# Kernel tuning notes

Hardware: AMD Instinct MI355X
Metric: run time of the kernel (lower is better)

## Reference

```python
import jax, jax.numpy as jnp
import numpy as np
from jax import lax

B, T, C = 8, 1025, 512
HEADS = 8
CACHE = 256          # int(dim * cache_ratio)
CLS = 1
L = 256              # gr_cache memory length
H = W = 32           # sqrt(T - CLS)
EPS = 1e-5


def setup_inputs() -> dict:
    key = jax.random.key(0)
    ks = jax.random.split(key, 40)
    def w(k, shape, scale=0.02):
        return jax.random.normal(k, shape, dtype=jnp.float32) * scale
    inp = {}
    inp['x'] = jax.random.normal(ks[0], (B, T, C), dtype=jnp.float32)
    inp['gr_cache'] = jax.random.normal(ks[1], (1, L, CACHE), dtype=jnp.float32)
    # self-attention (dim=512) params, weights stored (in, out)
    inp['Wq1'] = w(ks[2], (C, C)); inp['bq1'] = jnp.zeros((C,), jnp.float32)
    inp['Wk1'] = w(ks[3], (C, C)); inp['bk1'] = jnp.zeros((C,), jnp.float32)
    inp['Wv1'] = w(ks[4], (C, C)); inp['bv1'] = jnp.zeros((C,), jnp.float32)
    inp['Wo1'] = w(ks[5], (C, C)); inp['bo1'] = jnp.zeros((C,), jnp.float32)
    # memory attention (dim=cache_dim=256) params
    inp['Wq2'] = w(ks[6], (CACHE, CACHE)); inp['bq2'] = jnp.zeros((CACHE,), jnp.float32)
    inp['Wk2'] = w(ks[7], (CACHE, CACHE)); inp['bk2'] = jnp.zeros((CACHE,), jnp.float32)
    inp['Wv2'] = w(ks[8], (CACHE, CACHE)); inp['bv2'] = jnp.zeros((CACHE,), jnp.float32)
    inp['Wo2'] = w(ks[9], (CACHE, CACHE)); inp['bo2'] = jnp.zeros((CACHE,), jnp.float32)
    # GRU-style gate linears: in = 2*cache_dim, out = cache_dim
    inp['Wr'] = w(ks[10], (2 * CACHE, CACHE)); inp['br'] = jnp.zeros((CACHE,), jnp.float32)
    inp['Wz'] = w(ks[11], (2 * CACHE, CACHE)); inp['bz'] = jnp.zeros((CACHE,), jnp.float32)
    inp['Wa'] = w(ks[12], (2 * CACHE, CACHE)); inp['ba'] = jnp.zeros((CACHE,), jnp.float32)
    # LayerNorm(cache_dim)
    inp['gamma'] = jnp.ones((CACHE,), jnp.float32)
    inp['beta'] = jnp.zeros((CACHE,), jnp.float32)
    # per-head gate logits, init to -1 as in the module
    inp['lam'] = jnp.full((HEADS,), -1.0, dtype=jnp.float32)
    # grouped conv pos-emb: Conv2d(512, 512, k=3, groups=CACHE) -> (O=512, I/g=2, 3, 3)
    inp['conv_w'] = w(ks[13], (C, C // CACHE, 3, 3))
    inp['conv_b'] = jnp.zeros((C,), jnp.float32)
    return inp


def _mha(q_in, kv_in, Wq, bq, Wk, bk, Wv, bv, Wo, bo):
    Bq, Tq, D = q_in.shape
    Tk = kv_in.shape[1]
    dh = D // HEADS
    q = (q_in @ Wq + bq).reshape(Bq, Tq, HEADS, dh)
    k = (kv_in @ Wk + bk).reshape(Bq, Tk, HEADS, dh)
    v = (kv_in @ Wv + bv).reshape(Bq, Tk, HEADS, dh)
    s = jnp.einsum('bqhd,bkhd->bhqk', q, k) * (1.0 / np.sqrt(dh)).astype(np.float32)
    a = jax.nn.softmax(s, axis=-1)
    o = jnp.einsum('bhqk,bkhd->bqhd', a, v).reshape(Bq, Tq, D)
    return o @ Wo + bo


def reference(x, gr_cache, Wq1, bq1, Wk1, bk1, Wv1, bv1, Wo1, bo1,
              Wq2, bq2, Wk2, bk2, Wv2, bv2, Wo2, bo2,
              Wr, br, Wz, bz, Wa, ba, gamma, beta, lam, conv_w, conv_b):
    B_, T_, C_ = x.shape
    # ---- spatial positional embedding (faithful to torch view->permute quirk) ----
    tok = x[:, CLS:, :].reshape(B_, H, W, C_).transpose(0, 3, 1, 2)   # (B, C, H, W)
    pos = lax.conv_general_dilated(tok, conv_w, (1, 1), 'SAME',
                                   feature_group_count=CACHE,
                                   dimension_numbers=('NCHW', 'OIHW', 'NCHW'))
    pos = pos + conv_b[None, :, None, None]
    pos = pos.reshape(B_, C_, T_ - CLS).transpose(0, 2, 1)            # (B, T-1, C)
    pos = jnp.concatenate([jnp.zeros((B_, CLS, C_), pos.dtype), pos], axis=1)
    # ---- self attention ----
    x_self = _mha(x, x, Wq1, bq1, Wk1, bk1, Wv1, bv1, Wo1, bo1)       # (B, T, C)
    x_self_h = x_self.reshape(B_, T_, HEADS, C_ // HEADS)
    # ---- GRU-style gated cache update ----
    gr = jnp.broadcast_to(gr_cache, (B_, L, CACHE))
    x_summary = x_self[:, :, :CACHE]
    idx = (jnp.arange(L) * T_) // L                                   # nearest interpolate T -> L
    x_summary = x_summary[:, idx, :]                                  # (B, L, CACHE)
    cat = jnp.concatenate([gr, x_summary], axis=-1)
    reset = jax.nn.sigmoid(cat @ Wr + br)
    z = jax.nn.sigmoid(cat @ Wz + bz)
    cat2 = jnp.concatenate([reset * gr, x_summary], axis=-1)
    add = jax.nn.gelu(cat2 @ Wa + ba, approximate=False)
    mu = add.mean(-1, keepdims=True)
    var = ((add - mu) ** 2).mean(-1, keepdims=True)
    add = (add - mu) / jnp.sqrt(var + EPS) * gamma + beta             # LayerNorm
    gr_new = z * add + (1.0 - z) * gr
    # ---- memory attention on first cache_dim channels ----
    x_mem = _mha(x[:, :, :CACHE], gr_new, Wq2, bq2, Wk2, bk2, Wv2, bv2, Wo2, bo2)
    x_mem = x_mem.reshape(B_, T_, HEADS, CACHE // HEADS)
    # ---- per-head alpha blend with zero-padded mem branch ----
    alpha = jax.nn.sigmoid(lam).reshape(1, 1, HEADS, 1)
    pad = jnp.zeros((B_, T_, HEADS, (C_ - CACHE) // HEADS), x.dtype)
    out = (alpha * jnp.concatenate([x_mem, pad], axis=-1)
           + (1.0 - alpha) * x_self_h).reshape(B_, T_, C_) + pos
    return out
```

## Files before the change

kernel.cpp:

```cpp
#include <hip/hip_runtime.h>
#include <math.h>

typedef unsigned short u16;
typedef unsigned int u32;
typedef __attribute__((ext_vector_type(8))) short short8;
typedef __attribute__((ext_vector_type(4))) short short4v;
typedef __attribute__((ext_vector_type(4))) float f32x4;

constexpr int Bc = 8;
constexpr int Tt = 1025;
constexpr int Cc = 512;
constexpr int Hn = 8;
constexpr int CA = 256;
constexpr int Ll = 256;

#if __has_builtin(__builtin_amdgcn_exp2f)
#define EXP2F __builtin_amdgcn_exp2f
#else
#define EXP2F exp2f
#endif

__device__ __forceinline__ u16 f2bf(float f) {
  u32 u = __builtin_bit_cast(u32, f);
  u = (u + 0x7FFFu + ((u >> 16) & 1u)) >> 16;
  return (u16)u;
}
__device__ __forceinline__ u32 pack2f(float lo, float hi) {
  const u32 a = __builtin_bit_cast(u32, hi) + 0x8000u;
  const u32 b = __builtin_bit_cast(u32, lo) + 0x8000u;
  return __builtin_amdgcn_perm(a, b, 0x07060302u);
}

struct WC { const float* s; u16* d; int N; int tot; int kshift; };
struct WCP { WC w[11]; };

__global__ void wcast_k(WCP p) {
  const WC a = p.w[blockIdx.y];
  const int kmask = (1 << a.kshift) - 1;
  for (int idx = blockIdx.x * 256 + threadIdx.x; idx < a.tot; idx += gridDim.x * 256) {
    const int k = idx & kmask;
    const int n = idx >> a.kshift;
    a.d[idx] = f2bf(a.s[(size_t)k * a.N + n]);
  }
}

__global__ void xcast_k(const float* __restrict__ x, u16* __restrict__ xb, int n) {
  const int i = blockIdx.x * 256 + threadIdx.x;
  if (i < n) xb[i] = f2bf(x[i]);
}

enum { EP_NONE = 0, EP_SIGMOID = 1, EP_GELU = 2 };

template <int OUTBF, int ACT>
__global__ __launch_bounds__(256) void gemm_mfma(
    const u16* __restrict__ A, int lda,
    const u16* __restrict__ Wt,
    const float* __restrict__ bias,
    void* __restrict__ Cout,
    int M, int N, int K, float oscale)
{
  __shared__ u16 As[128][32];
  __shared__ u16 Bs[128][32];
  const int tid = threadIdx.x;
  const int m0 = blockIdx.y * 128, n0 = blockIdx.x * 128;
  const int ln = tid & 15, quad = (tid >> 4) & 3, wv = tid >> 6;
  const int wm = (wv & 1) * 64, wn = (wv >> 1) * 64;
  const int sr = tid >> 1;
  const int sk = (tid & 1) * 16;

  f32x4 zf = {0.f, 0.f, 0.f, 0.f};
  f32x4 acc[4][4];
  #pragma unroll
  for (int i = 0; i < 4; i++)
    #pragma unroll
    for (int j = 0; j < 4; j++) acc[i][j] = zf;

  const short8 z8 = {0, 0, 0, 0, 0, 0, 0, 0};

  for (int k0 = 0; k0 < K; k0 += 32) {
    const int gm = m0 + sr;
    short8 a0 = z8, a1 = z8;
    if (gm < M) {
      const u16* p = A + (size_t)gm * lda + k0 + sk;
      a0 = *(const short8*)p;
      a1 = *(const short8*)(p + 8);
    }
    *(short8*)&As[sr][sk] = a0;
    *(short8*)&As[sr][sk + 8] = a1;
    {
      const u16* q = Wt + (size_t)(n0 + sr) * K + k0 + sk;
      *(short8*)&Bs[sr][sk] = *(const short8*)q;
      *(short8*)&Bs[sr][sk + 8] = *(const short8*)(q + 8);
    }
    __syncthreads();

    short8 af[4], bf[4];
    #pragma unroll
    for (int i = 0; i < 4; i++) af[i] = *(const short8*)&As[wm + i * 16 + ln][quad * 8];
    #pragma unroll
    for (int j = 0; j < 4; j++) bf[j] = *(const short8*)&Bs[wn + j * 16 + ln][quad * 8];
    #pragma unroll
    for (int i = 0; i < 4; i++)
      #pragma unroll
      for (int j = 0; j < 4; j++)
        acc[i][j] = __builtin_amdgcn_mfma_f32_16x16x32_bf16(af[i], bf[j], acc[i][j], 0, 0, 0);
    __syncthreads();
  }

  float bj[4];
  #pragma unroll
  for (int j = 0; j < 4; j++) bj[j] = bias[n0 + wn + j * 16 + ln];

  #pragma unroll
  for (int i = 0; i < 4; i++) {
    #pragma unroll
    for (int r = 0; r < 4; r++) {
      const int gm = m0 + wm + i * 16 + quad * 4 + r;
      if (gm >= M) continue;
      #pragma unroll
      for (int j = 0; j < 4; j++) {
        float v = (acc[i][j][r] + bj[j]) * oscale;
        if (ACT == EP_SIGMOID)   v = 1.f / (1.f + __expf(-v));
        else if (ACT == EP_GELU) v = 0.5f * v * (1.f + erff(v * 0.70710678118654752f));
        const size_t off = (size_t)gm * N + n0 + wn + j * 16 + ln;
        if (OUTBF) ((u16*)Cout)[off] = f2bf(v);
        else       ((float*)Cout)[off] = v;
      }
    }
  }
}

template <int DH>
__global__ __launch_bounds__(128) void attn_mfma(
    const u16* __restrict__ Qp, const u16* __restrict__ Kp,
    const u16* __restrict__ Vp, u16* __restrict__ Op,
    int Tq, int Tk, int qbs, int kbs)
{
  constexpr int RS = Hn * DH;
  constexpr int MK = DH / 8 - 1;
  constexpr int NC = DH / 32;
  constexpr int NM = DH / 16;

  __shared__ u16 Ks[32 * DH];
  __shared__ u16 Vt[DH * 32];
  __shared__ u16 Pb[2 * 32 * 32];

  const int b = blockIdx.y >> 3, h = blockIdx.y & 7;
  const int q0 = blockIdx.x * 64;
  const int tid = threadIdx.x;
  const int wv = tid >> 6;
  const int lane = tid & 63;
  const int ln = lane & 15, quad = lane >> 4;

  const u16* Qb = Qp + (size_t)b * qbs + h * DH;
  const u16* Kb = Kp + (size_t)b * kbs + h * DH;
  const u16* Vb = Vp + (size_t)b * kbs + h * DH;
  u16* Ob = Op + (size_t)b * qbs + h * DH;

  const short8 z8 = {0, 0, 0, 0, 0, 0, 0, 0};
  const f32x4 zf = {0.f, 0.f, 0.f, 0.f};

  short8 qf[2][NC];
  #pragma unroll
  for (int qs = 0; qs < 2; qs++) {
    const int gq = q0 + wv * 32 + qs * 16 + ln;
    #pragma unroll
    for (int c = 0; c < NC; c++) {
      if (gq < Tq) qf[qs][c] = *(const short8*)(Qb + (size_t)gq * RS + c * 32 + quad * 8);
      else         qf[qs][c] = z8;
    }
  }

  f32x4 oacc[2][NM];
  float lsum[2] = {0.f, 0.f};
  #pragma unroll
  for (int qs = 0; qs < 2; qs++)
    #pragma unroll
    for (int c = 0; c < NM; c++) oacc[qs][c] = zf;

  const int nfull = Tk >> 5;
  const int nit = (Tk + 31) >> 5;

  for (int it = 0; it < nit; it++) {
    const int k0 = it << 5;
    const bool full = (it < nfull);
    __syncthreads();

    {
      const int r = tid >> 2;
      const int gk = k0 + r;
      if (DH == 64) {
        const u16* p = Kb + (size_t)gk * RS + (tid & 3) * 16;
        short8 a = z8, b2 = z8;
        if (full || gk < Tk) { a = *(const short8*)p; b2 = *(const short8*)(p + 8); }
        const int g0 = (((tid & 3) * 2) ^ (r & 7));
        const int g1 = (((tid & 3) * 2 + 1) ^ (r & 7));
        *(short8*)&Ks[r * 64 + g0 * 8] = a;
        *(short8*)&Ks[r * 64 + g1 * 8] = b2;
      } else {
        const u16* p = Kb + (size_t)gk * RS + (tid & 3) * 8;
        short8 a = z8;
        if (full || gk < Tk) a = *(const short8*)p;
        const int g0 = ((tid & 3) ^ (r & 3));
        *(short8*)&Ks[r * 32 + g0 * 8] = a;
      }
    }
    {
      const int vd0 = (tid & 15) * (DH / 16);
      const int vk = (tid >> 4) * 4;
      const int gb = vk >> 3, off = vk & 7;
      short4v vrow[4];
      #pragma unroll
      for (int i2 = 0; i2 < 4; i2++) {
        const int gk = k0 + vk + i2;
        short4v t = {0, 0, 0, 0};
        if (DH == 64) {
          if (full || gk < Tk) t = *(const short4v*)(Vb + (size_t)gk * RS + vd0);
        } else {
          if (full || gk < Tk) {
            ushort2 u = *(const ushort2*)(Vb + (size_t)gk * RS + vd0);
            t[0] = (short)u.x; t[1] = (short)u.y;
          }
        }
        vrow[i2] = t;
      }
      #pragma unroll
      for (int i = 0; i < DH / 16; i++) {
        const int d = vd0 + i;
        const int h2 = (d ^ (d >> 3)) & 3;
        short4v w = {vrow[0][i], vrow[1][i], vrow[2][i], vrow[3][i]};
        *(short4v*)&Vt[d * 32 + ((gb ^ h2) << 3) + off] = w;
      }
    }
    __syncthreads();

    short8 kf[2][NC];
    #pragma unroll
    for (int kc = 0; kc < 2; kc++) {
      const int r = kc * 16 + ln;
      #pragma unroll
      for (int c = 0; c < NC; c++) {
        const int g = (4 * c + quad) ^ (r & MK);
        kf[kc][c] = *(const short8*)&Ks[r * DH + g * 8];
      }
    }

    #pragma unroll
    for (int qs = 0; qs < 2; qs++) {
      #pragma unroll
      for (int kc = 0; kc < 2; kc++) {
        f32x4 s = zf;
        #pragma unroll
        for (int c = 0; c < NC; c++)
          s = __builtin_amdgcn_mfma_f32_16x16x32_bf16(kf[kc][c], qf[qs][c], s, 0, 0, 0);
        float p0, p1, p2, p3;
        if (full) {
          p0 = EXP2F(s[0]); p1 = EXP2F(s[1]); p2 = EXP2F(s[2]); p3 = EXP2F(s[3]);
        } else {
          const int kb = k0 + kc * 16 + quad * 4;
          p0 = (kb + 0 < Tk) ? EXP2F(s[0]) : 0.f;
          p1 = (kb + 1 < Tk) ? EXP2F(s[1]) : 0.f;
          p2 = (kb + 2 < Tk) ? EXP2F(s[2]) : 0.f;
          p3 = (kb + 3 < Tk) ? EXP2F(s[3]) : 0.f;
        }
        lsum[qs] += (p0 + p1) + (p2 + p3);
        short4v pw;
        ((u32*)&pw)[0] = pack2f(p0, p1);
        ((u32*)&pw)[1] = pack2f(p2, p3);
        const int q = qs * 16 + ln;
        const int g = ((kc * 2 + (quad >> 1)) ^ (ln & 3)) & 3;
        *(short4v*)&Pb[wv * 1024 + q * 32 + (g << 3) + (quad & 1) * 4] = pw;
      }
    }

    short8 pf2[2];
    #pragma unroll
    for (int qs = 0; qs < 2; qs++) {
      const int q = qs * 16 + ln;
      const int g = quad ^ (ln & 3);
      pf2[qs] = *(const short8*)&Pb[wv * 1024 + q * 32 + g * 8];
    }
    #pragma unroll
    for (int c = 0; c < NM; c++) {
      const int d = c * 16 + ln;
      const int g = quad ^ ((d ^ (d >> 3)) & 3);
      const short8 vf = *(const short8*)&Vt[d * 32 + g * 8];
      #pragma unroll
      for (int qs = 0; qs < 2; qs++)
        oacc[qs][c] = __builtin_amdgcn_mfma_f32_16x16x32_bf16(pf2[qs], vf, oacc[qs][c], 0, 0, 0);
    }
  }

  float lq[2];
  #pragma unroll
  for (int qs = 0; qs < 2; qs++) {
    float t = lsum[qs];
    t += __shfl_xor(t, 16);
    t += __shfl_xor(t, 32);
    lq[qs] = t;
  }
  #pragma unroll
  for (int qs = 0; qs < 2; qs++) {
    #pragma unroll
    for (int r = 0; r < 4; r++) {
      const float linv = 1.f / __shfl(lq[qs], quad * 4 + r);
      const int gq = q0 + wv * 32 + qs * 16 + quad * 4 + r;
      if (gq >= Tq) continue;
      #pragma unroll
      for (int c = 0; c < NM; c++)
        Ob[(size_t)gq * RS + c * 16 + ln] = f2bf(oacc[qs][c][r] * linv);
    }
  }
}

__global__ __launch_bounds__(256) void conv_combine(
    const float* __restrict__ x, const float* __restrict__ cw,
    const float* __restrict__ cb, const float* __restrict__ x_self,
    const float* __restrict__ x_mem, const float* __restrict__ lam,
    float* __restrict__ out)
{
  const int bh = blockIdx.x;
  const int b = bh >> 5, hh = bh & 31;
  const int c = (blockIdx.y << 8) + threadIdx.x;
  const int ci = c & ~1;
  const int dd = c & 63;
  const int h8 = c >> 6;
  const float alpha = 1.f / (1.f + __expf(-lam[h8]));
  const float bias = cb[c];

  float wgt[2][9];
  #pragma unroll
  for (int ch = 0; ch < 2; ch++)
    #pragma unroll
    for (int k = 0; k < 9; k++) wgt[ch][k] = cw[c * 18 + ch * 9 + k];

  const float* xrow[3];
  bool rv[3];
  #pragma unroll
  for (int r = 0; r < 3; r++) {
    const int h2 = hh + r - 1;
    rv[r] = (unsigned)h2 < 32u;
    xrow[r] = x + ((size_t)(b * Tt) + 1 + h2 * 32) * Cc + ci;
  }

  float2 win[3][3];
  #pragma unroll
  for (int r = 0; r < 3; r++) {
    win[r][0] = make_float2(0.f, 0.f);
    win[r][1] = rv[r] ? *(const float2*)(xrow[r]) : make_float2(0.f, 0.f);
  }

  const size_t bT = (size_t)b * Tt;
  for (int w = 0; w < 32; w++) {
    #pragma unroll
    for (int r = 0; r < 3; r++)
      win[r][2] = (rv[r] && w + 1 < 32) ? *(const float2*)(xrow[r] + (w + 1) * Cc)
                                        : make_float2(0.f, 0.f);
    float pos = bias;
    #pragma unroll
    for (int r = 0; r < 3; r++)
      #pragma unroll
      for (int col = 0; col < 3; col++) {
        pos += win[r][col].x * wgt[0][r * 3 + col];
        pos += win[r][col].y * wgt[1][r * 3 + col];
      }
    const size_t bt = bT + 1 + hh * 32 + w;
    const float mem = (dd < 32) ? x_mem[bt * 256 + h8 * 32 + dd] : 0.f;
    out[bt * 512 + c] = pos + alpha * mem + (1.f - alpha) * x_self[bt * 512 + c];
    #pragma unroll
    for (int r = 0; r < 3; r++) { win[r][0] = win[r][1]; win[r][1] = win[r][2]; }
  }

  if (hh == 0) {
    const float mem = (dd < 32) ? x_mem[bT * 256 + h8 * 32 + dd] : 0.f;
    out[bT * 512 + c] = alpha * mem + (1.f - alpha) * x_self[bT * 512 + c];
  }
}

__global__ void build_cat(const float* __restrict__ gr_cache,
                          const float* __restrict__ x_self,
                          u16* __restrict__ cat)
{
  const int idx = blockIdx.x * 256 + threadIdx.x;
  if (idx >= Bc * Ll * 512) return;
  const int k = idx & 511;
  const int bi = idx >> 9;
  const int i = bi & 255;
  const int b = bi >> 8;
  float v;
  if (k < 256) v = gr_cache[i * 256 + k];
  else         v = x_self[((size_t)(b * Tt + 4 * i)) * Cc + (k - 256)];
  cat[idx] = f2bf(v);
}

__global__ void build_cat2(const float* __restrict__ gr_cache,
                           const float* __restrict__ reset,
                           u16* __restrict__ cat)
{
  const int idx = blockIdx.x * 256 + threadIdx.x;
  if (idx >= Bc * Ll * 256) return;
  const int k = idx & 255;
  const int bi = idx >> 8;
  const int i = bi & 255;
  cat[(size_t)bi * 512 + k] = f2bf(gr_cache[i * 256 + k] * reset[idx]);
}

__device__ inline float block_sum256(float v, float* red)
{
  #pragma unroll
  for (int o = 32; o >= 1; o >>= 1) v += __shfl_down(v, o);
  const int wid = threadIdx.x >> 6;
  if ((threadIdx.x & 63) == 0) red[wid] = v;
  __syncthreads();
  const float t = red[0] + red[1] + red[2] + red[3];
  __syncthreads();
  return t;
}

__global__ __launch_bounds__(256) void ln_gate(
    const float* __restrict__ add_raw, const float* __restrict__ z,
    const float* __restrict__ gr_cache, const float* __restrict__ gamma,
    const float* __restrict__ beta, u16* __restrict__ gr_new)
{
  __shared__ float red[4];
  const int bi = blockIdx.x;
  const int i = bi & 255;
  const int c = threadIdx.x;
  const float v = add_raw[(size_t)bi * 256 + c];
  const float mu = block_sum256(v, red) * (1.f / 256.f);
  const float dv = v - mu;
  const float var = block_sum256(dv * dv, red) * (1.f / 256.f);
  const float nrm = dv * rsqrtf(var + 1e-5f) * gamma[c] + beta[c];
  const float zz = z[(size_t)bi * 256 + c];
  gr_new[(size_t)bi * 256 + c] = f2bf(zz * nrm + (1.f - zz) * gr_cache[i * 256 + c]);
}

extern "C" void kernel_launch(void* const* d_in, const int* in_sizes, int n_in,
                              void* d_out, int out_size, void* d_ws, size_t ws_size,
                              hipStream_t stream)
{
  const float* x        = (const float*)d_in[0];
  const float* gr_cache = (const float*)d_in[1];
  const float* Wq1 = (const float*)d_in[2];  const float* bq1 = (const float*)d_in[3];
  const float* Wk1 = (const float*)d_in[4];  const float* bk1 = (const float*)d_in[5];
  const float* Wv1 = (const float*)d_in[6];  const float* bv1 = (const float*)d_in[7];
  const float* Wo1 = (const float*)d_in[8];  const float* bo1 = (const float*)d_in[9];
  const float* Wq2 = (const float*)d_in[10]; const float* bq2 = (const float*)d_in[11];
  const float* Wk2 = (const float*)d_in[12]; const float* bk2 = (const float*)d_in[13];
  const float* Wv2 = (const float*)d_in[14]; const float* bv2 = (const float*)d_in[15];
  const float* Wo2 = (const float*)d_in[16]; const float* bo2 = (const float*)d_in[17];
  const float* Wr  = (const float*)d_in[18]; const float* br  = (const float*)d_in[19];
  const float* Wz  = (const float*)d_in[20]; const float* bz  = (const float*)d_in[21];
  const float* Wa  = (const float*)d_in[22]; const float* ba  = (const float*)d_in[23];
  const float* gamma = (const float*)d_in[24];
  const float* beta  = (const float*)d_in[25];
  const float* lam   = (const float*)d_in[26];
  const float* conv_w = (const float*)d_in[27];
  const float* conv_b = (const float*)d_in[28];
  float* out = (float*)d_out;

  const int M1 = Bc * Tt;
  const int M2 = Bc * Ll;
  const size_t BTC = (size_t)Bc * Tt * Cc;
  const size_t BLA = (size_t)Bc * Ll * CA;
  const size_t BL2 = (size_t)Bc * Ll * 512;

  char* W = (char*)d_ws;
  u16*   xb     = (u16*)(W + 0);
  u16*   q1     = (u16*)(W + 8396800);
  u16*   k1     = (u16*)(W + 16793600);
  u16*   v1     = (u16*)(W + 25190400);
  u16*   att1   = (u16*)(W + 33587200);
  float* x_self = (float*)(W + 41984000);
  u16*   wtb    = (u16*)(W + 58777600);
  u16*   cat    = (u16*)(W + 8396800);
  float* rg     = (float*)(W + 10493952);
  float* zg     = (float*)(W + 12591104);
  float* addr_  = (float*)(W + 14688256);
  u16*   gr_new = (u16*)(W + 16785408);
  u16*   k2     = (u16*)(W + 17833984);
  u16*   v2     = (u16*)(W + 18882560);
  u16*   q2     = (u16*)(W + 19931136);
  u16*   att2   = (u16*)(W + 24129536);
  float* x_mem  = (float*)(W + 28327936);

  u16* Wq1t = wtb + 0;       u16* Wk1t = wtb + 262144;  u16* Wv1t = wtb + 524288;
  u16* Wo1t = wtb + 786432;  u16* Wrt  = wtb + 1048576; u16* Wzt  = wtb + 1179648;
  u16* Wat  = wtb + 1310720; u16* Wq2t = wtb + 1441792; u16* Wk2t = wtb + 1507328;
  u16* Wv2t = wtb + 1572864; u16* Wo2t = wtb + 1638400;

  const dim3 blk(256);
  const int ew_btc = (int)((BTC + 255) / 256);

  {
    WCP p;
    const float* ws_[11] = {Wq1, Wk1, Wv1, Wo1, Wr, Wz, Wa, Wq2, Wk2, Wv2, Wo2};
    u16* wd_[11] = {Wq1t, Wk1t, Wv1t, Wo1t, Wrt, Wzt, Wat, Wq2t, Wk2t, Wv2t, Wo2t};
    const int Kk[11] = {512,512,512,512,512,512,512,256,256,256,256};
    const int Nn[11] = {512,512,512,512,256,256,256,256,256,256,256};
    for (int i = 0; i < 11; i++) {
      p.w[i].s = ws_[i]; p.w[i].d = wd_[i]; p.w[i].N = Nn[i];
      p.w[i].tot = Kk[i] * Nn[i];
      p.w[i].kshift = (Kk[i] == 512) ? 9 : 8;
    }
    wcast_k<<<dim3(64, 11), blk, 0, stream>>>(p);
  }
  xcast_k<<<ew_btc, blk, 0, stream>>>(x, xb, (int)BTC);

  const dim3 g512(4, 65), g256m1(2, 65), g256m2(2, 16);
  gemm_mfma<1, EP_NONE><<<g512, blk, 0, stream>>>(xb, 512, Wq1t, bq1, q1, M1, 512, 512,
                                                  0.18033688011112042f);
  gemm_mfma<1, EP_NONE><<<g512, blk, 0, stream>>>(xb, 512, Wk1t, bk1, k1, M1, 512, 512, 1.f);
  gemm_mfma<1, EP_NONE><<<g512, blk, 0, stream>>>(xb, 512, Wv1t, bv1, v1, M1, 512, 512, 1.f);
  attn_mfma<64><<<dim3(17, 64), dim3(128), 0, stream>>>(q1, k1, v1, att1, Tt, Tt,
                                                        Tt * 512, Tt * 512);
  gemm_mfma<0, EP_NONE><<<g512, blk, 0, stream>>>(att1, 512, Wo1t, bo1, x_self, M1, 512, 512, 1.f);

  build_cat<<<(int)((BL2 + 255) / 256), blk, 0, stream>>>(gr_cache, x_self, cat);
  gemm_mfma<0, EP_SIGMOID><<<g256m2, blk, 0, stream>>>(cat, 512, Wrt, br, rg, M2, 256, 512, 1.f);
  gemm_mfma<0, EP_SIGMOID><<<g256m2, blk, 0, stream>>>(cat, 512, Wzt, bz, zg, M2, 256, 512, 1.f);
  build_cat2<<<(int)((BLA + 255) / 256), blk, 0, stream>>>(gr_cache, rg, cat);
  gemm_mfma<0, EP_GELU><<<g256m2, blk, 0, stream>>>(cat, 512, Wat, ba, addr_, M2, 256, 512, 1.f);
  ln_gate<<<M2, blk, 0, stream>>>(addr_, zg, gr_cache, gamma, beta, gr_new);

  gemm_mfma<1, EP_NONE><<<g256m1, blk, 0, stream>>>(xb, 512, Wq2t, bq2, q2, M1, 256, 256,
                                                    0.25503490664918414f);
  gemm_mfma<1, EP_NONE><<<g256m2, blk, 0, stream>>>(gr_new, 256, Wk2t, bk2, k2, M2, 256, 256, 1.f);
  gemm_mfma<1, EP_NONE><<<g256m2, blk, 0, stream>>>(gr_new, 256, Wv2t, bv2, v2, M2, 256, 256, 1.f);
  attn_mfma<32><<<dim3(17, 64), dim3(128), 0, stream>>>(q2, k2, v2, att2, Tt, Ll,
                                                        Tt * 256, Ll * 256);
  gemm_mfma<0, EP_NONE><<<g256m1, blk, 0, stream>>>(att2, 256, Wo2t, bo2, x_mem, M1, 256, 256, 1.f);

  conv_combine<<<dim3(Bc * 32, 2), blk, 0, stream>>>(x, conv_w, conv_b, x_self,
                                                     x_mem, lam, out);
}
```

Before: 397.2 us.

## Fuse QKV/Q2, R/Z, K2/V2 GEMMs; cast x in-GEMM; drop K smem staging

```diff
diff --git a/kernel.cpp b/kernel.cpp
--- a/kernel.cpp
+++ b/kernel.cpp
@@ -31,7 +31,7 @@
   return __builtin_amdgcn_perm(a, b, 0x07060302u);
 }
 
-struct WC { const float* s; u16* d; int N; int tot; int kshift; };
+struct WC { const float* s; u16* d; int sN; int sK; int kshift; int tot; };
 struct WCP { WC w[11]; };
 
 __global__ void wcast_k(WCP p) {
@@ -40,24 +40,26 @@
   for (int idx = blockIdx.x * 256 + threadIdx.x; idx < a.tot; idx += gridDim.x * 256) {
     const int k = idx & kmask;
     const int n = idx >> a.kshift;
-    a.d[idx] = f2bf(a.s[(size_t)k * a.N + n]);
-  }
-}
-
-__global__ void xcast_k(const float* __restrict__ x, u16* __restrict__ xb, int n) {
-  const int i = blockIdx.x * 256 + threadIdx.x;
-  if (i < n) xb[i] = f2bf(x[i]);
+    a.d[idx] = (k < a.sK) ? f2bf(a.s[(size_t)k * a.sN + n]) : (u16)0;
+  }
 }
 
 enum { EP_NONE = 0, EP_SIGMOID = 1, EP_GELU = 2 };
 
-template <int OUTBF, int ACT>
+struct GemmEpi {
+  const float* bias[4];
+  int start[4];
+  float scale[4];
+  int nreg;
+};
+
+template <int AF32, int OUTBF, int ACT>
 __global__ __launch_bounds__(256) void gemm_mfma(
-    const u16* __restrict__ A, int lda,
+    const void* __restrict__ Av, int lda,
     const u16* __restrict__ Wt,
-    const float* __restrict__ bias,
+    GemmEpi epi,
     void* __restrict__ Cout,
-    int M, int N, int K, float oscale)
+    int M, int N, int K)
 {
   __shared__ u16 As[128][32];
   __shared__ u16 Bs[128][32];
@@ -81,9 +83,25 @@
     const int gm = m0 + sr;
     short8 a0 = z8, a1 = z8;
     if (gm < M) {
-      const u16* p = A + (size_t)gm * lda + k0 + sk;
-      a0 = *(const short8*)p;
-      a1 = *(const short8*)(p + 8);
+      if (AF32) {
+        const float* p = (const float*)Av + (size_t)gm * lda + k0 + sk;
+        const float4 f0 = *(const float4*)(p + 0);
+        const float4 f1 = *(const float4*)(p + 4);
+        const float4 f2 = *(const float4*)(p + 8);
+        const float4 f3 = *(const float4*)(p + 12);
+        ((u32*)&a0)[0] = pack2f(f0.x, f0.y);
+        ((u32*)&a0)[1] = pack2f(f0.z, f0.w);
+        ((u32*)&a0)[2] = pack2f(f1.x, f1.y);
+        ((u32*)&a0)[3] = pack2f(f1.z, f1.w);
+        ((u32*)&a1)[0] = pack2f(f2.x, f2.y);
+        ((u32*)&a1)[1] = pack2f(f2.z, f2.w);
+        ((u32*)&a1)[2] = pack2f(f3.x, f3.y);
+        ((u32*)&a1)[3] = pack2f(f3.z, f3.w);
+      } else {
+        const u16* p = (const u16*)Av + (size_t)gm * lda + k0 + sk;
+        a0 = *(const short8*)p;
+        a1 = *(const short8*)(p + 8);
+      }
     }
     *(short8*)&As[sr][sk] = a0;
     *(short8*)&As[sr][sk + 8] = a1;
@@ -107,9 +125,16 @@
     __syncthreads();
   }
 
+  int ri = 0;
+  #pragma unroll
+  for (int i = 1; i < 4; i++)
+    if (i < epi.nreg && epi.start[i] <= n0) ri = i;
+  const float* bp = epi.bias[ri] - epi.start[ri];
+  const float sc = epi.scale[ri];
+
   float bj[4];
   #pragma unroll
-  for (int j = 0; j < 4; j++) bj[j] = bias[n0 + wn + j * 16 + ln];
+  for (int j = 0; j < 4; j++) bj[j] = bp[n0 + wn + j * 16 + ln];
 
   #pragma unroll
   for (int i = 0; i < 4; i++) {
@@ -119,7 +144,7 @@
       if (gm >= M) continue;
       #pragma unroll
       for (int j = 0; j < 4; j++) {
-        float v = (acc[i][j][r] + bj[j]) * oscale;
+        float v = (acc[i][j][r] + bj[j]) * sc;
         if (ACT == EP_SIGMOID)   v = 1.f / (1.f + __expf(-v));
         else if (ACT == EP_GELU) v = 0.5f * v * (1.f + erff(v * 0.70710678118654752f));
         const size_t off = (size_t)gm * N + n0 + wn + j * 16 + ln;
@@ -134,15 +159,12 @@
 __global__ __launch_bounds__(128) void attn_mfma(
     const u16* __restrict__ Qp, const u16* __restrict__ Kp,
     const u16* __restrict__ Vp, u16* __restrict__ Op,
-    int Tq, int Tk, int qbs, int kbs)
-{
-  constexpr int RS = Hn * DH;
-  constexpr int MK = DH / 8 - 1;
+    int Tq, int Tk, int qbs, int kbs, int obs, int qrs, int krs, int ors)
+{
   constexpr int NC = DH / 32;
   constexpr int NM = DH / 16;
 
-  __shared__ u16 Ks[32 * DH];
-  __shared__ u16 Vt[DH * 32];
+  __shared__ u16 Vt[2][DH * 32];
   __shared__ u16 Pb[2 * 32 * 32];
 
   const int b = blockIdx.y >> 3, h = blockIdx.y & 7;
@@ -155,7 +177,7 @@
   const u16* Qb = Qp + (size_t)b * qbs + h * DH;
   const u16* Kb = Kp + (size_t)b * kbs + h * DH;
   const u16* Vb = Vp + (size_t)b * kbs + h * DH;
-  u16* Ob = Op + (size_t)b * qbs + h * DH;
+  u16* Ob = Op + (size_t)b * obs + h * DH;
 
   const short8 z8 = {0, 0, 0, 0, 0, 0, 0, 0};
   const f32x4 zf = {0.f, 0.f, 0.f, 0.f};
@@ -166,7 +188,7 @@
     const int gq = q0 + wv * 32 + qs * 16 + ln;
     #pragma unroll
     for (int c = 0; c < NC; c++) {
-      if (gq < Tq) qf[qs][c] = *(const short8*)(Qb + (size_t)gq * RS + c * 32 + quad * 8);
+      if (gq < Tq) qf[qs][c] = *(const short8*)(Qb + (size_t)gq * qrs + c * 32 + quad * 8);
       else         qf[qs][c] = z8;
     }
   }
@@ -177,6 +199,10 @@
   for (int qs = 0; qs < 2; qs++)
     #pragma unroll
     for (int c = 0; c < NM; c++) oacc[qs][c] = zf;
+
+  const int vd0 = (tid & 15) * (DH / 16);
+  const int vk = (tid >> 4) * 4;
+  const int gb = vk >> 3, off = vk & 7;
 
   const int nfull = Tk >> 5;
   const int nit = (Tk + 31) >> 5;
@@ -184,41 +210,39 @@
   for (int it = 0; it < nit; it++) {
     const int k0 = it << 5;
     const bool full = (it < nfull);
-    __syncthreads();
+    u16* vt = &Vt[it & 1][0];
+
+    short8 kf[2][NC];
+    if (full) {
+      #pragma unroll
+      for (int kc = 0; kc < 2; kc++)
+        #pragma unroll
+        for (int c = 0; c < NC; c++)
+          kf[kc][c] = *(const short8*)(Kb + (size_t)(k0 + kc * 16 + ln) * krs
+                                          + c * 32 + quad * 8);
+    } else {
+      #pragma unroll
+      for (int kc = 0; kc < 2; kc++)
+        #pragma unroll
+        for (int c = 0; c < NC; c++) {
+          const int row = k0 + kc * 16 + ln;
+          kf[kc][c] = (row < Tk)
+              ? *(const short8*)(Kb + (size_t)row * krs + c * 32 + quad * 8)
+              : z8;
+        }
+    }
 
     {
-      const int r = tid >> 2;
-      const int gk = k0 + r;
-      if (DH == 64) {
-        const u16* p = Kb + (size_t)gk * RS + (tid & 3) * 16;
-        short8 a = z8, b2 = z8;
-        if (full || gk < Tk) { a = *(const short8*)p; b2 = *(const short8*)(p + 8); }
-        const int g0 = (((tid & 3) * 2) ^ (r & 7));
-        const int g1 = (((tid & 3) * 2 + 1) ^ (r & 7));
-        *(short8*)&Ks[r * 64 + g0 * 8] = a;
-        *(short8*)&Ks[r * 64 + g1 * 8] = b2;
-      } else {
-        const u16* p = Kb + (size_t)gk * RS + (tid & 3) * 8;
-        short8 a = z8;
-        if (full || gk < Tk) a = *(const short8*)p;
-        const int g0 = ((tid & 3) ^ (r & 3));
-        *(short8*)&Ks[r * 32 + g0 * 8] = a;
-      }
-    }
-    {
-      const int vd0 = (tid & 15) * (DH / 16);
-      const int vk = (tid >> 4) * 4;
-      const int gb = vk >> 3, off = vk & 7;
       short4v vrow[4];
       #pragma unroll
       for (int i2 = 0; i2 < 4; i2++) {
         const int gk = k0 + vk + i2;
         short4v t = {0, 0, 0, 0};
         if (DH == 64) {
-          if (full || gk < Tk) t = *(const short4v*)(Vb + (size_t)gk * RS + vd0);
+          if (full || gk < Tk) t = *(const short4v*)(Vb + (size_t)gk * krs + vd0);
         } else {
           if (full || gk < Tk) {
-            ushort2 u = *(const ushort2*)(Vb + (size_t)gk * RS + vd0);
+            ushort2 u = *(const ushort2*)(Vb + (size_t)gk * krs + vd0);
             t[0] = (short)u.x; t[1] = (short)u.y;
           }
         }
@@ -229,21 +253,10 @@
         const int d = vd0 + i;
         const int h2 = (d ^ (d >> 3)) & 3;
         short4v w = {vrow[0][i], vrow[1][i], vrow[2][i], vrow[3][i]};
-        *(short4v*)&Vt[d * 32 + ((gb ^ h2) << 3) + off] = w;
+        *(short4v*)&vt[d * 32 + ((gb ^ h2) << 3) + off] = w;
       }
     }
     __syncthreads();
-
-    short8 kf[2][NC];
-    #pragma unroll
-    for (int kc = 0; kc < 2; kc++) {
-      const int r = kc * 16 + ln;
-      #pragma unroll
-      for (int c = 0; c < NC; c++) {
-        const int g = (4 * c + quad) ^ (r & MK);
-        kf[kc][c] = *(const short8*)&Ks[r * DH + g * 8];
-      }
-    }
 
     #pragma unroll
     for (int qs = 0; qs < 2; qs++) {
@@ -284,7 +297,7 @@
     for (int c = 0; c < NM; c++) {
       const int d = c * 16 + ln;
       const int g = quad ^ ((d ^ (d >> 3)) & 3);
-      const short8 vf = *(const short8*)&Vt[d * 32 + g * 8];
+      const short8 vf = *(const short8*)&vt[d * 32 + g * 8];
       #pragma unroll
       for (int qs = 0; qs < 2; qs++)
         oacc[qs][c] = __builtin_amdgcn_mfma_f32_16x16x32_bf16(pf2[qs], vf, oacc[qs][c], 0, 0, 0);
@@ -308,7 +321,7 @@
       if (gq >= Tq) continue;
       #pragma unroll
       for (int c = 0; c < NM; c++)
-        Ob[(size_t)gq * RS + c * 16 + ln] = f2bf(oacc[qs][c][r] * linv);
+        Ob[(size_t)gq * ors + c * 16 + ln] = f2bf(oacc[qs][c][r] * linv);
     }
   }
 }
@@ -394,7 +407,7 @@
 }
 
 __global__ void build_cat2(const float* __restrict__ gr_cache,
-                           const float* __restrict__ reset,
+                           const float* __restrict__ rzg,
                            u16* __restrict__ cat)
 {
   const int idx = blockIdx.x * 256 + threadIdx.x;
@@ -402,7 +415,7 @@
   const int k = idx & 255;
   const int bi = idx >> 8;
   const int i = bi & 255;
-  cat[(size_t)bi * 512 + k] = f2bf(gr_cache[i * 256 + k] * reset[idx]);
+  cat[(size_t)bi * 512 + k] = f2bf(gr_cache[i * 256 + k] * rzg[(size_t)bi * 512 + k]);
 }
 
 __device__ inline float block_sum256(float v, float* red)
@@ -418,7 +431,7 @@
 }
 
 __global__ __launch_bounds__(256) void ln_gate(
-    const float* __restrict__ add_raw, const float* __restrict__ z,
+    const float* __restrict__ add_raw, const float* __restrict__ rzg,
     const float* __restrict__ gr_cache, const float* __restrict__ gamma,
     const float* __restrict__ beta, u16* __restrict__ gr_new)
 {
@@ -431,7 +444,7 @@
   const float dv = v - mu;
   const float var = block_sum256(dv * dv, red) * (1.f / 256.f);
   const float nrm = dv * rsqrtf(var + 1e-5f) * gamma[c] + beta[c];
-  const float zz = z[(size_t)bi * 256 + c];
+  const float zz = rzg[(size_t)bi * 512 + 256 + c];
   gr_new[(size_t)bi * 256 + c] = f2bf(zz * nrm + (1.f - zz) * gr_cache[i * 256 + c]);
 }
 
@@ -466,70 +479,102 @@
   const size_t BL2 = (size_t)Bc * Ll * 512;
 
   char* W = (char*)d_ws;
-  u16*   xb     = (u16*)(W + 0);
-  u16*   q1     = (u16*)(W + 8396800);
-  u16*   k1     = (u16*)(W + 16793600);
-  u16*   v1     = (u16*)(W + 25190400);
-  u16*   att1   = (u16*)(W + 33587200);
-  float* x_self = (float*)(W + 41984000);
-  u16*   wtb    = (u16*)(W + 58777600);
-  u16*   cat    = (u16*)(W + 8396800);
-  float* rg     = (float*)(W + 10493952);
-  float* zg     = (float*)(W + 12591104);
-  float* addr_  = (float*)(W + 14688256);
-  u16*   gr_new = (u16*)(W + 16785408);
-  u16*   k2     = (u16*)(W + 17833984);
-  u16*   v2     = (u16*)(W + 18882560);
-  u16*   q2     = (u16*)(W + 19931136);
-  u16*   att2   = (u16*)(W + 24129536);
-  float* x_mem  = (float*)(W + 28327936);
-
-  u16* Wq1t = wtb + 0;       u16* Wk1t = wtb + 262144;  u16* Wv1t = wtb + 524288;
-  u16* Wo1t = wtb + 786432;  u16* Wrt  = wtb + 1048576; u16* Wzt  = wtb + 1179648;
-  u16* Wat  = wtb + 1310720; u16* Wq2t = wtb + 1441792; u16* Wk2t = wtb + 1507328;
-  u16* Wv2t = wtb + 1572864; u16* Wo2t = wtb + 1638400;
+  u16*   qkvq  = (u16*)(W + 0);
+  u16*   att1  = (u16*)(W + 29388800);
+  u16*   att2  = (u16*)(W + 29388800);
+  float* x_self= (float*)(W + 37785600);
+  u16*   cat   = (u16*)(W + 54579200);
+  float* rzg   = (float*)(W + 56676352);
+  float* addr_ = (float*)(W + 60870656);
+  float* x_mem = (float*)(W + 54579200);
+  u16*   gr_new= (u16*)(W + 62976000);
+  u16*   k2v2  = (u16*)(W + 64024576);
+  u16*   wtb   = (u16*)(W + 66121728);
+
+  u16* megaW = wtb;
+  u16* o1W   = wtb + 917504;
+  u16* rzW   = wtb + 1179648;
+  u16* aW    = wtb + 1441792;
+  u16* kvW   = wtb + 1572864;
+  u16* o2W   = wtb + 1703936;
 
   const dim3 blk(256);
-  const int ew_btc = (int)((BTC + 255) / 256);
 
   {
     WCP p;
-    const float* ws_[11] = {Wq1, Wk1, Wv1, Wo1, Wr, Wz, Wa, Wq2, Wk2, Wv2, Wo2};
-    u16* wd_[11] = {Wq1t, Wk1t, Wv1t, Wo1t, Wrt, Wzt, Wat, Wq2t, Wk2t, Wv2t, Wo2t};
-    const int Kk[11] = {512,512,512,512,512,512,512,256,256,256,256};
-    const int Nn[11] = {512,512,512,512,256,256,256,256,256,256,256};
-    for (int i = 0; i < 11; i++) {
-      p.w[i].s = ws_[i]; p.w[i].d = wd_[i]; p.w[i].N = Nn[i];
-      p.w[i].tot = Kk[i] * Nn[i];
-      p.w[i].kshift = (Kk[i] == 512) ? 9 : 8;
-    }
+    p.w[0]  = {Wq1, megaW + 0,           512, 512, 9, 512 * 512};
+    p.w[1]  = {Wk1, megaW + 512 * 512,   512, 512, 9, 512 * 512};
+    p.w[2]  = {Wv1, megaW + 1024 * 512,  512, 512, 9, 512 * 512};
+    p.w[3]  = {Wq2, megaW + 1536 * 512,  256, 256, 9, 256 * 512};
+    p.w[4]  = {Wo1, o1W,                 512, 512, 9, 512 * 512};
+    p.w[5]  = {Wr,  rzW + 0,             256, 512, 9, 256 * 512};
+    p.w[6]  = {Wz,  rzW + 256 * 512,     256, 512, 9, 256 * 512};
+    p.w[7]  = {Wa,  aW,                  256, 512, 9, 256 * 512};
+    p.w[8]  = {Wk2, kvW + 0,             256, 256, 8, 256 * 256};
+    p.w[9]  = {Wv2, kvW + 256 * 256,     256, 256, 8, 256 * 256};
+    p.w[10] = {Wo2, o2W,                 256, 256, 8, 256 * 256};
     wcast_k<<<dim3(64, 11), blk, 0, stream>>>(p);
   }
-  xcast_k<<<ew_btc, blk, 0, stream>>>(x, xb, (int)BTC);
-
-  const dim3 g512(4, 65), g256m1(2, 65), g256m2(2, 16);
-  gemm_mfma<1, EP_NONE><<<g512, blk, 0, stream>>>(xb, 512, Wq1t, bq1, q1, M1, 512, 512,
-                                                  0.18033688011112042f);
-  gemm_mfma<1, EP_NONE><<<g512, blk, 0, stream>>>(xb, 512, Wk1t, bk1, k1, M1, 512, 512, 1.f);
-  gemm_mfma<1, EP_NONE><<<g512, blk, 0, stream>>>(xb, 512, Wv1t, bv1, v1, M1, 512, 512, 1.f);
-  attn_mfma<64><<<dim3(17, 64), dim3(128), 0, stream>>>(q1, k1, v1, att1, Tt, Tt,
-                                                        Tt * 512, Tt * 512);
-  gemm_mfma<0, EP_NONE><<<g512, blk, 0, stream>>>(att1, 512, Wo1t, bo1, x_self, M1, 512, 512, 1.f);
+
+  const float sQ1 = 0.18033688011112042f;
+  const float sQ2 = 0.25503490664918414f;
+
+  {
+    GemmEpi e;
+    e.bias[0] = bq1; e.start[0] = 0;    e.scale[0] = sQ1;
+    e.bias[1] = bk1; e.start[1] = 512;  e.scale[1] = 1.f;
+    e.bias[2] = bv1; e.start[2] = 1024; e.scale[2] = 1.f;
+    e.bias[3] = bq2; e.start[3] = 1536; e.scale[3] = sQ2;
+    e.nreg = 4;
+    gemm_mfma<1, 1, EP_NONE><<<dim3(14, 65), blk, 0, stream>>>(
+        x, 512, megaW, e, qkvq, M1, 1792, 512);
+  }
+
+  attn_mfma<64><<<dim3(17, 64), dim3(128), 0, stream>>>(
+      qkvq, qkvq + 512, qkvq + 1024, att1, Tt, Tt,
+      Tt * 1792, Tt * 1792, Tt * 512, 1792, 1792, 512);
+
+  {
+    GemmEpi e; e.bias[0] = bo1; e.start[0] = 0; e.scale[0] = 1.f; e.nreg = 1;
+    gemm_mfma<0, 0, EP_NONE><<<dim3(4, 65), blk, 0, stream>>>(
+        att1, 512, o1W, e, x_self, M1, 512, 512);
+  }
 
   build_cat<<<(int)((BL2 + 255) / 256), blk, 0, stream>>>(gr_cache, x_self, cat);
-  gemm_mfma<0, EP_SIGMOID><<<g256m2, blk, 0, stream>>>(cat, 512, Wrt, br, rg, M2, 256, 512, 1.f);
-  gemm_mfma<0, EP_SIGMOID><<<g256m2, blk, 0, stream>>>(cat, 512, Wzt, bz, zg, M2, 256, 512, 1.f);
-  build_cat2<<<(int)((BLA + 255) / 256), blk, 0, stream>>>(gr_cache, rg, cat);
-  gemm_mfma<0, EP_GELU><<<g256m2, blk, 0, stream>>>(cat, 512, Wat, ba, addr_, M2, 256, 512, 1.f);
-  ln_gate<<<M2, blk, 0, stream>>>(addr_, zg, gr_cache, gamma, beta, gr_new);
-
-  gemm_mfma<1, EP_NONE><<<g256m1, blk, 0, stream>>>(xb, 512, Wq2t, bq2, q2, M1, 256, 256,
-                                                    0.25503490664918414f);
-  gemm_mfma<1, EP_NONE><<<g256m2, blk, 0, stream>>>(gr_new, 256, Wk2t, bk2, k2, M2, 256, 256, 1.f);
-  gemm_mfma<1, EP_NONE><<<g256m2, blk, 0, stream>>>(gr_new, 256, Wv2t, bv2, v2, M2, 256, 256, 1.f);
-  attn_mfma<32><<<dim3(17, 64), dim3(128), 0, stream>>>(q2, k2, v2, att2, Tt, Ll,
-                                                        Tt * 256, Ll * 256);
-  gemm_mfma<0, EP_NONE><<<g256m1, blk, 0, stream>>>(att2, 256, Wo2t, bo2, x_mem, M1, 256, 256, 1.f);
+  {
+    GemmEpi e;
+    e.bias[0] = br; e.start[0] = 0;   e.scale[0] = 1.f;
+    e.bias[1] = bz; e.start[1] = 256; e.scale[1] = 1.f;
+    e.nreg = 2;
+    gemm_mfma<0, 0, EP_SIGMOID><<<dim3(4, 16), blk, 0, stream>>>(
+        cat, 512, rzW, e, rzg, M2, 512, 512);
+  }
+  build_cat2<<<(int)((BLA + 255) / 256), blk, 0, stream>>>(gr_cache, rzg, cat);
+  {
+    GemmEpi e; e.bias[0] = ba; e.start[0] = 0; e.scale[0] = 1.f; e.nreg = 1;
+    gemm_mfma<0, 0, EP_GELU><<<dim3(2, 16), blk, 0, stream>>>(
+        cat, 512, aW, e, addr_, M2, 256, 512);
+  }
+  ln_gate<<<M2, blk, 0, stream>>>(addr_, rzg, gr_cache, gamma, beta, gr_new);
+
+  {
+    GemmEpi e;
+    e.bias[0] = bk2; e.start[0] = 0;   e.scale[0] = 1.f;
+    e.bias[1] = bv2; e.start[1] = 256; e.scale[1] = 1.f;
+    e.nreg = 2;
+    gemm_mfma<0, 1, EP_NONE><<<dim3(4, 16), blk, 0, stream>>>(
+        gr_new, 256, kvW, e, k2v2, M2, 512, 256);
+  }
+
+  attn_mfma<32><<<dim3(17, 64), dim3(128), 0, stream>>>(
+      qkvq + 1536, k2v2, k2v2 + 256, att2, Tt, Ll,
+      Tt * 1792, Ll * 512, Tt * 256, 1792, 512, 256);
+
+  {
+    GemmEpi e; e.bias[0] = bo2; e.start[0] = 0; e.scale[0] = 1.f; e.nreg = 1;
+    gemm_mfma<0, 0, EP_NONE><<<dim3(2, 65), blk, 0, stream>>>(
+        att2, 256, o2W, e, x_mem, M1, 256, 256);
+  }
 
   conv_combine<<<dim3(Bc * 32, 2), blk, 0, stream>>>(x, conv_w, conv_b, x_self,
                                                      x_mem, lam, out);
```

New measurement: 370.3 us. 6.8% less time.
